# Kernel tuning notes

Measured on AMD Instinct MI355X. Metric: run time of the kernel, lower is better.

The kernel has to match this reference:

```python
import jax, jax.numpy as jnp
from jax import lax
import numpy as np

INPUT_SIZE = 2
HIDDEN_SIZE = 64
OUTPUT_SIZE = 2
SEQ_LEN = 1024
BATCH = 512


def setup_inputs() -> dict:
    key = jax.random.key(0)
    ks = jax.random.split(key, 7)
    H, I, O = HIDDEN_SIZE, INPUT_SIZE, OUTPUT_SIZE
    s = 1.0 / np.sqrt(H)  # PyTorch LSTM/Linear init scale
    x = jax.random.normal(ks[0], (SEQ_LEN, BATCH, I), dtype=jnp.float32)
    W_ih = jax.random.uniform(ks[1], (4 * H, I), minval=-s, maxval=s, dtype=jnp.float32)
    W_hh = jax.random.uniform(ks[2], (4 * H, H), minval=-s, maxval=s, dtype=jnp.float32)
    b_ih = jax.random.uniform(ks[3], (4 * H,), minval=-s, maxval=s, dtype=jnp.float32)
    b_hh = jax.random.uniform(ks[4], (4 * H,), minval=-s, maxval=s, dtype=jnp.float32)
    W_fc = jax.random.uniform(ks[5], (O, H), minval=-s, maxval=s, dtype=jnp.float32)
    b_fc = jax.random.uniform(ks[6], (O,), minval=-s, maxval=s, dtype=jnp.float32)
    return {"x": x, "W_ih": W_ih, "W_hh": W_hh, "b_ih": b_ih, "b_hh": b_hh,
            "W_fc": W_fc, "b_fc": b_fc}


def reference(x, W_ih, W_hh, b_ih, b_hh, W_fc, b_fc):
    # x: [T, B, I] (torch nn.LSTM default batch_first=False)
    T, B, _ = x.shape
    H = W_hh.shape[1]
    b = b_ih + b_hh  # [4H]

    def step(carry, xt):
        h, c = carry  # [B, H] each
        gates = xt @ W_ih.T + h @ W_hh.T + b  # [B, 4H]
        i, f, g, o = jnp.split(gates, 4, axis=-1)  # PyTorch gate order i,f,g,o
        i = jax.nn.sigmoid(i)
        f = jax.nn.sigmoid(f)
        g = jnp.tanh(g)
        o = jax.nn.sigmoid(o)
        c_new = f * c + i * g
        h_new = o * jnp.tanh(c_new)
        return (h_new, c_new), h_new

    h0 = jnp.zeros((B, H), dtype=x.dtype)
    c0 = jnp.zeros((B, H), dtype=x.dtype)
    _, hs = lax.scan(step, (h0, c0), x)  # hs: [T, B, H]

    # Faithful to torch: out[:, -1, :] with out shape [T, B, H] selects the
    # LAST BATCH element's hidden state at every timestep -> [T, H].
    last = hs[:, -1, :]
    return last @ W_fc.T + b_fc  # [T, O]
```

## Files before the change

### kernel.cpp

```cpp
#include <hip/hip_runtime.h>


#define T_LEN 1024
#define BATCH 512
#define HID   64

__device__ __forceinline__ float fast_rcp(float x) {
    return __builtin_amdgcn_rcpf(x);
}
__device__ __forceinline__ float fast_sigmoid(float x) {
    return fast_rcp(1.0f + __expf(-x));
}
__device__ __forceinline__ float fast_tanh(float x) {
    return 1.0f - 2.0f * fast_rcp(__expf(2.0f * x) + 1.0f);
}

__global__ __launch_bounds__(256, 1)
void lstm_seq_kernel(const float* __restrict__ x,
                     const float* __restrict__ W_ih,
                     const float* __restrict__ W_hh,
                     const float* __restrict__ b_ih,
                     const float* __restrict__ b_hh,
                     const float* __restrict__ W_fc,
                     const float* __restrict__ b_fc,
                     float* __restrict__ out,
                     float* __restrict__ hist)
{
    __shared__ float xs[2 * T_LEN];
    __shared__ float gbuf[2 * 256];
    __shared__ float hbuf[4][2][HID];
    __shared__ float hring[64 * HID];

    const int tid  = threadIdx.x;
    const int lane = tid & 63;
    const int gate = tid >> 6;
    const int row  = tid;

    for (int j = 0; j < 4; ++j) {
        int t = tid + j * 256;
        const float2 v = *(const float2*)(x + (size_t)(t * BATCH + (BATCH - 1)) * 2);
        xs[2 * t]     = v.x;
        xs[2 * t + 1] = v.y;
    }

    float w[HID];
    {
        const float4* wr = (const float4*)(W_hh + row * HID);
        #pragma unroll
        for (int k = 0; k < HID / 4; ++k) {
            float4 v = wr[k];
            w[4*k+0] = v.x; w[4*k+1] = v.y; w[4*k+2] = v.z; w[4*k+3] = v.w;
        }
    }
    const float bsum = b_ih[row] + b_hh[row];
    const float wi0  = W_ih[row * 2 + 0];
    const float wi1  = W_ih[row * 2 + 1];

    float hval = 0.0f;
    float cval = 0.0f;

    hbuf[gate][0][lane] = 0.0f;

    __syncthreads();

    for (int t = 0; t < T_LEN; ++t) {
        const float4* hb = (const float4*)&hbuf[gate][t & 1][0];
        float4 hv[16];
        #pragma unroll
        for (int j = 0; j < 16; ++j) hv[j] = hb[j];

        const float2 xv = *(const float2*)(xs + 2 * t);
        float a0 = fmaf(wi0, xv.x, bsum);
        float a1 = wi1 * xv.y;
        float a2 = 0.0f, a3 = 0.0f;
        #pragma unroll
        for (int j = 0; j < 16; ++j) {
            a0 = fmaf(w[4*j+0], hv[j].x, a0);
            a1 = fmaf(w[4*j+1], hv[j].y, a1);
            a2 = fmaf(w[4*j+2], hv[j].z, a2);
            a3 = fmaf(w[4*j+3], hv[j].w, a3);
        }
        const float acc = (a0 + a1) + (a2 + a3);
        const float act = (gate == 2) ? fast_tanh(acc) : fast_sigmoid(acc);

        const int gb = (t & 1) * 256;
        gbuf[gb + row] = act;
        __syncthreads();

        const float gi = gbuf[gb + lane];
        const float gf = gbuf[gb + 64 + lane];
        const float gg = gbuf[gb + 128 + lane];
        const float go = gbuf[gb + 192 + lane];
        cval = fmaf(gf, cval, gi * gg);
        hval = go * fast_tanh(cval);

        hbuf[gate][(t + 1) & 1][lane] = hval;

        if (gate == 0) {
            hring[(t & 63) * HID + lane] = hval;
            if ((t & 63) == 63) {
                float4*       dst = (float4*)(hist + (t - 63) * HID);
                const float4* src = (const float4*)hring;
                #pragma unroll
                for (int j = 0; j < 16; ++j)
                    dst[lane + 64 * j] = src[lane + 64 * j];
            }
        }
    }

    __syncthreads();

    #pragma unroll
    for (int j = 0; j < 8; ++j) {
        const int idx = tid + j * 256;
        const int t   = idx >> 1;
        const int o   = idx & 1;
        const float4* hv4 = (const float4*)(hist + t * HID);
        const float4* wv  = (const float4*)(W_fc + o * HID);
        float p0 = 0.f, p1 = 0.f, p2 = 0.f, p3 = 0.f;
        #pragma unroll
        for (int k = 0; k < HID / 4; ++k) {
            float4 h4 = hv4[k], w4 = wv[k];
            p0 = fmaf(h4.x, w4.x, p0);
            p1 = fmaf(h4.y, w4.y, p1);
            p2 = fmaf(h4.z, w4.z, p2);
            p3 = fmaf(h4.w, w4.w, p3);
        }
        out[idx] = b_fc[o] + ((p0 + p1) + (p2 + p3));
    }
}

extern "C" void kernel_launch(void* const* d_in, const int* in_sizes, int n_in,
                              void* d_out, int out_size, void* d_ws, size_t ws_size,
                              hipStream_t stream) {
    const float* x    = (const float*)d_in[0];
    const float* W_ih = (const float*)d_in[1];
    const float* W_hh = (const float*)d_in[2];
    const float* b_ih = (const float*)d_in[3];
    const float* b_hh = (const float*)d_in[4];
    const float* W_fc = (const float*)d_in[5];
    const float* b_fc = (const float*)d_in[6];
    float* out  = (float*)d_out;
    float* hist = (float*)d_ws;

    lstm_seq_kernel<<<dim3(1), dim3(256), 0, stream>>>(
        x, W_ih, W_hh, b_ih, b_hh, W_fc, b_fc, out, hist);
}
```

Measured before the change: 553.7 us.

## Collapse LSTM recurrence into a single wavefront using readlane broadcasts

```diff
diff --git a/kernel.cpp b/kernel.cpp
--- a/kernel.cpp
+++ b/kernel.cpp
@@ -1,5 +1,7 @@
 #include <hip/hip_runtime.h>
 
+
+typedef float f32x2 __attribute__((ext_vector_type(2)));
 
 #define T_LEN 1024
 #define BATCH 512
@@ -15,7 +17,7 @@
     return 1.0f - 2.0f * fast_rcp(__expf(2.0f * x) + 1.0f);
 }
 
-__global__ __launch_bounds__(256, 1)
+__global__ __launch_bounds__(64, 1)
 void lstm_seq_kernel(const float* __restrict__ x,
                      const float* __restrict__ W_ih,
                      const float* __restrict__ W_hh,
@@ -27,92 +29,88 @@
                      float* __restrict__ hist)
 {
     __shared__ float xs[2 * T_LEN];
-    __shared__ float gbuf[2 * 256];
-    __shared__ float hbuf[4][2][HID];
-    __shared__ float hring[64 * HID];
 
-    const int tid  = threadIdx.x;
-    const int lane = tid & 63;
-    const int gate = tid >> 6;
-    const int row  = tid;
+    const int lane = threadIdx.x;
 
-    for (int j = 0; j < 4; ++j) {
-        int t = tid + j * 256;
+    for (int j = 0; j < 16; ++j) {
+        const int t = lane + 64 * j;
         const float2 v = *(const float2*)(x + (size_t)(t * BATCH + (BATCH - 1)) * 2);
         xs[2 * t]     = v.x;
         xs[2 * t + 1] = v.y;
     }
 
-    float w[HID];
+    f32x2 w0[32], w1[32], w2[32], w3[32];
     {
-        const float4* wr = (const float4*)(W_hh + row * HID);
+        const float4* r0 = (const float4*)(W_hh + (0 * HID + lane) * HID);
+        const float4* r1 = (const float4*)(W_hh + (1 * HID + lane) * HID);
+        const float4* r2 = (const float4*)(W_hh + (2 * HID + lane) * HID);
+        const float4* r3 = (const float4*)(W_hh + (3 * HID + lane) * HID);
         #pragma unroll
-        for (int k = 0; k < HID / 4; ++k) {
-            float4 v = wr[k];
-            w[4*k+0] = v.x; w[4*k+1] = v.y; w[4*k+2] = v.z; w[4*k+3] = v.w;
+        for (int k = 0; k < 16; ++k) {
+            float4 v;
+            v = r0[k]; w0[2*k] = (f32x2){v.x, v.y}; w0[2*k+1] = (f32x2){v.z, v.w};
+            v = r1[k]; w1[2*k] = (f32x2){v.x, v.y}; w1[2*k+1] = (f32x2){v.z, v.w};
+            v = r2[k]; w2[2*k] = (f32x2){v.x, v.y}; w2[2*k+1] = (f32x2){v.z, v.w};
+            v = r3[k]; w3[2*k] = (f32x2){v.x, v.y}; w3[2*k+1] = (f32x2){v.z, v.w};
         }
     }
-    const float bsum = b_ih[row] + b_hh[row];
-    const float wi0  = W_ih[row * 2 + 0];
-    const float wi1  = W_ih[row * 2 + 1];
+    const float wi00 = W_ih[(0 * HID + lane) * 2 + 0], wi01 = W_ih[(0 * HID + lane) * 2 + 1];
+    const float wi10 = W_ih[(1 * HID + lane) * 2 + 0], wi11 = W_ih[(1 * HID + lane) * 2 + 1];
+    const float wi20 = W_ih[(2 * HID + lane) * 2 + 0], wi21 = W_ih[(2 * HID + lane) * 2 + 1];
+    const float wi30 = W_ih[(3 * HID + lane) * 2 + 0], wi31 = W_ih[(3 * HID + lane) * 2 + 1];
+    const float bs0 = b_ih[0 * HID + lane] + b_hh[0 * HID + lane];
+    const float bs1 = b_ih[1 * HID + lane] + b_hh[1 * HID + lane];
+    const float bs2 = b_ih[2 * HID + lane] + b_hh[2 * HID + lane];
+    const float bs3 = b_ih[3 * HID + lane] + b_hh[3 * HID + lane];
 
     float hval = 0.0f;
     float cval = 0.0f;
 
-    hbuf[gate][0][lane] = 0.0f;
+    for (int t = 0; t < T_LEN; ++t) {
+        const float2 xv = *(const float2*)(xs + 2 * t);
 
-    __syncthreads();
+        const int hb = __float_as_int(hval);
+        f32x2 acc0 = (f32x2){0.0f, 0.0f};
+        f32x2 acc1 = acc0, acc2 = acc0, acc3 = acc0;
 
-    for (int t = 0; t < T_LEN; ++t) {
-        const float4* hb = (const float4*)&hbuf[gate][t & 1][0];
-        float4 hv[16];
+        int hs[16];
         #pragma unroll
-        for (int j = 0; j < 16; ++j) hv[j] = hb[j];
+        for (int b = 0; b < 4; ++b) {
+            #pragma unroll
+            for (int k = 0; k < 16; ++k)
+                hs[k] = __builtin_amdgcn_readlane(hb, 16 * b + k);
+            __builtin_amdgcn_sched_barrier(0);
+            #pragma unroll
+            for (int p = 0; p < 8; ++p) {
+                f32x2 hp;
+                hp.x = __int_as_float(hs[2 * p]);
+                hp.y = __int_as_float(hs[2 * p + 1]);
+                const int i = 8 * b + p;
+                acc0 += w0[i] * hp;
+                acc1 += w1[i] * hp;
+                acc2 += w2[i] * hp;
+                acc3 += w3[i] * hp;
+            }
+        }
 
-        const float2 xv = *(const float2*)(xs + 2 * t);
-        float a0 = fmaf(wi0, xv.x, bsum);
-        float a1 = wi1 * xv.y;
-        float a2 = 0.0f, a3 = 0.0f;
-        #pragma unroll
-        for (int j = 0; j < 16; ++j) {
-            a0 = fmaf(w[4*j+0], hv[j].x, a0);
-            a1 = fmaf(w[4*j+1], hv[j].y, a1);
-            a2 = fmaf(w[4*j+2], hv[j].z, a2);
-            a3 = fmaf(w[4*j+3], hv[j].w, a3);
-        }
-        const float acc = (a0 + a1) + (a2 + a3);
-        const float act = (gate == 2) ? fast_tanh(acc) : fast_sigmoid(acc);
+        float p0 = (acc0.x + acc0.y) + fmaf(wi00, xv.x, fmaf(wi01, xv.y, bs0));
+        float p1 = (acc1.x + acc1.y) + fmaf(wi10, xv.x, fmaf(wi11, xv.y, bs1));
+        float p2 = (acc2.x + acc2.y) + fmaf(wi20, xv.x, fmaf(wi21, xv.y, bs2));
+        float p3 = (acc3.x + acc3.y) + fmaf(wi30, xv.x, fmaf(wi31, xv.y, bs3));
 
-        const int gb = (t & 1) * 256;
-        gbuf[gb + row] = act;
-        __syncthreads();
+        const float gi = fast_sigmoid(p0);
+        const float gf = fast_sigmoid(p1);
+        const float gg = fast_tanh(p2);
+        const float go = fast_sigmoid(p3);
 
-        const float gi = gbuf[gb + lane];
-        const float gf = gbuf[gb + 64 + lane];
-        const float gg = gbuf[gb + 128 + lane];
-        const float go = gbuf[gb + 192 + lane];
         cval = fmaf(gf, cval, gi * gg);
         hval = go * fast_tanh(cval);
 
-        hbuf[gate][(t + 1) & 1][lane] = hval;
-
-        if (gate == 0) {
-            hring[(t & 63) * HID + lane] = hval;
-            if ((t & 63) == 63) {
-                float4*       dst = (float4*)(hist + (t - 63) * HID);
-                const float4* src = (const float4*)hring;
-                #pragma unroll
-                for (int j = 0; j < 16; ++j)
-                    dst[lane + 64 * j] = src[lane + 64 * j];
-            }
-        }
+        hist[t * HID + lane] = hval;
     }
 
-    __syncthreads();
-
-    #pragma unroll
-    for (int j = 0; j < 8; ++j) {
-        const int idx = tid + j * 256;
+    for (int j = 0; j < 32; ++j) {
+        const int idx = lane + 64 * j;
         const int t   = idx >> 1;
         const int o   = idx & 1;
         const float4* hv4 = (const float4*)(hist + t * HID);
@@ -143,6 +141,6 @@
     float* out  = (float*)d_out;
     float* hist = (float*)d_ws;
 
-    lstm_seq_kernel<<<dim3(1), dim3(256), 0, stream>>>(
+    lstm_seq_kernel<<<dim3(1), dim3(64), 0, stream>>>(
         x, W_ih, W_hh, b_ih, b_hh, W_fc, b_fc, out, hist);
 }
```

Measured after the change: 603.3 us. 9.0% more time.
